# Kernel optimization log

Hardware: AMD Instinct MI355X
Metric: run time of the kernel (lower is better)

## Reference

```python
import jax, jax.numpy as jnp
import numpy as np

B, F, D, H, P, V = 2048, 64, 128, 8, 64, 100000


def setup_inputs() -> dict:
    key = jax.random.key(0)
    ks = jax.random.split(key, 8)
    xavier = lambda k, shape: jax.random.uniform(
        k, shape, jnp.float32, -1.0, 1.0) * np.sqrt(6.0 / (shape[0] + shape[1]))
    return {
        "feat_index": jax.random.randint(ks[0], (B, F), 0, V),
        "emb_table": xavier(ks[1], (V, D)),
        "Wq": xavier(ks[2], (D, H * P)),
        "Wk": xavier(ks[3], (D, H * P)),
        "Wv": xavier(ks[4], (D, H * P)),
        "Wr": xavier(ks[5], (D, H * P)),
        "out_w": xavier(ks[6], (F * H * P, 1)),
        "out_b": jnp.zeros((1,), jnp.float32),
    }


def reference(feat_index, emb_table, Wq, Wk, Wv, Wr, out_w, out_b):
    e = emb_table[feat_index]                                   # [B, F, D]
    # project and split heads: [B, F, H*P] -> [B, H, F, P]
    split = lambda t: t.reshape(B, F, H, P).transpose(0, 2, 1, 3)
    q = split(jnp.einsum('bfd,de->bfe', e, Wq))
    k = split(jnp.einsum('bfd,de->bfe', e, Wk))
    v = split(jnp.einsum('bfd,de->bfe', e, Wv))
    scores = jnp.einsum('bhqp,bhkp->bhqk', q, k)                # [B, H, F, F]
    # NOTE: original applies softmax over dim=2 (the query axis), faithfully kept
    att = jax.nn.softmax(scores, axis=2)
    av = jnp.einsum('bhqk,bhkp->bhqp', att, v)                  # [B, H, F, P]
    # split over heads then cat on last dim == transpose heads next to P
    multi = av.transpose(0, 2, 1, 3).reshape(B, F, H * P)       # [B, F, H*P]
    res = jnp.einsum('bfd,de->bfe', e, Wr)
    multi = jax.nn.relu(multi + res)
    flat = multi.reshape(B, F * H * P)
    y = jax.nn.sigmoid(flat @ out_w + out_b)                    # [B, 1]
    return y
```

## Files before the change

### kernel.cpp

```cpp
#include <hip/hip_runtime.h>
#include <hip/hip_bf16.h>
#include <hip/hip_fp8.h>
#include <stdint.h>


typedef __attribute__((ext_vector_type(8))) __bf16 bf16x8;
typedef __attribute__((ext_vector_type(4))) float f32x4;
typedef __attribute__((ext_vector_type(2))) long long llx2;

#define LDP 72
#define E_SCALE 64.0f
#define W_SCALE 8.0f
#define INV_RAW (1.0f / 512.0f)
#define INV_RAW2 (1.0f / (512.0f * 512.0f))

#define SWZ(row, col) (((row) * 64) + ((col) ^ (((row) & 7) << 3)))

__device__ inline unsigned short f2bf(float f) {
    unsigned u = __float_as_uint(f);
    return (unsigned short)((u + 0x7fff + ((u >> 16) & 1)) >> 16);
}
__device__ inline unsigned short f2bf_t(float f) {
    return (unsigned short)(__float_as_uint(f) >> 16);
}
__device__ inline unsigned pack_bf2(float a, float b) {
#if __has_builtin(__builtin_amdgcn_cvt_pk_bf16_f32)
    typedef __attribute__((ext_vector_type(2))) __bf16 bf16x2;
    bf16x2 r = __builtin_amdgcn_cvt_pk_bf16_f32(a, b);
    return *(unsigned*)&r;
#else
    return (__float_as_uint(a) >> 16) | (__float_as_uint(b) & 0xFFFF0000u);
#endif
}
__device__ inline unsigned pack_fp8x4(float a, float b, float c, float d) {
#if __has_builtin(__builtin_amdgcn_cvt_pk_fp8_f32)
    int u = __builtin_amdgcn_cvt_pk_fp8_f32(a, b, 0, false);
    u = __builtin_amdgcn_cvt_pk_fp8_f32(c, d, u, true);
    return (unsigned)u;
#else
    __hip_fp8_e4m3 qa(a), qb(b), qc(c), qd(d);
    return (unsigned)qa.__x | ((unsigned)qb.__x << 8) |
           ((unsigned)qc.__x << 16) | ((unsigned)qd.__x << 24);
#endif
}

__global__ __launch_bounds__(256) void prep_w(
        const float* __restrict__ Wq, const float* __restrict__ Wk,
        const float* __restrict__ Wv, const float* __restrict__ Wr,
        const float* __restrict__ out_w,
        unsigned char* __restrict__ Wt, float* __restrict__ ow2) {
    int blk = blockIdx.x;
    if (blk >= 256) {
        int i = (blk - 256) * 256 + threadIdx.x;
        int f = i & 63;
        int hp = i >> 6;
        ow2[i] = out_w[(size_t)f * 512 + hp];
        return;
    }
    __shared__ float t[64][20];
    int mat = blk >> 6;
    int dt8 = (blk >> 3) & 7;
    int ct  = blk & 7;
    const float* W = (mat == 0) ? Wq : (mat == 1) ? Wk : (mat == 2) ? Wv : Wr;
    int tid  = threadIdx.x;
    int col  = tid & 63;
    int row0 = tid >> 6;
    for (int i = 0; i < 4; i++) {
        int row = row0 + i * 4;
        t[col][row] = W[(size_t)(dt8 * 16 + row) * 512 + ct * 64 + col];
    }
    __syncthreads();
    int wc  = tid & 63;
    int seg = tid >> 6;
    unsigned u = pack_fp8x4(t[wc][seg * 4 + 0] * W_SCALE, t[wc][seg * 4 + 1] * W_SCALE,
                            t[wc][seg * 4 + 2] * W_SCALE, t[wc][seg * 4 + 3] * W_SCALE);
    int d0 = dt8 * 16 + seg * 4;
    int q_ = (d0 >> 3) & 3, k_ = d0 >> 5, r_ = d0 & 7;
    *(unsigned*)&Wt[((size_t)mat * 512 + ct * 64 + wc) * 128 + q_ * 32 + k_ * 8 + r_] = u;
}

__global__ __launch_bounds__(256, 2) void autoint_kernel(
        const int* __restrict__ fidx,
        const float* __restrict__ emb,
        const unsigned char* __restrict__ Wt,
        const float* __restrict__ ow2,
        const float* __restrict__ out_b,
        float* __restrict__ y) {
    __shared__ __align__(16) unsigned short smem[4 * 64 * 64];
    unsigned short* q_lds   = smem;
    unsigned short* k_lds   = smem + 4096;
    unsigned short* vT_lds  = smem + 2 * 4096;
    unsigned short* att_lds = smem + 3 * 4096;
    unsigned char*  smem8   = (unsigned char*)smem;

    const int b    = blockIdx.x;
    const int tid  = threadIdx.x;
    const int wave = tid >> 6;
    const int lane = tid & 63;
    const int quad = lane >> 4;
    const int ln16 = lane & 15;

    const int* idx = fidx + b * 64;

    for (int it = 0; it < 4; it++) {
        int s  = tid + it * 256;
        int tm = s >> 8, ks = (s >> 6) & 3, qd = (s >> 4) & 3, m = s & 15;
        int f  = tm * 16 + m;
        const float* src = emb + (size_t)idx[f] * 128 + ks * 32 + qd * 8;
        float4 lo = *(const float4*)src;
        float4 hi = *(const float4*)(src + 4);
        uint2 pk;
        pk.x = pack_fp8x4(lo.x * E_SCALE, lo.y * E_SCALE, lo.z * E_SCALE, lo.w * E_SCALE);
        pk.y = pack_fp8x4(hi.x * E_SCALE, hi.y * E_SCALE, hi.z * E_SCALE, hi.w * E_SCALE);
        *(uint2*)&smem8[s * 8] = pk;
    }
    __syncthreads();

    long long a[4][4];
    for (int tm = 0; tm < 4; tm++)
        for (int ks = 0; ks < 4; ks++)
            a[tm][ks] = *(const long long*)&smem8[((tm * 4 + ks) * 64 + lane) * 8];
    __syncthreads();

    float acc_out = 0.f;

    auto loadW = [&](int m, int h, long long (&bf)[4]) {
        const unsigned char* WtM =
            Wt + ((size_t)m * 512 + h * 64 + wave * 16 + ln16) * 128 + quad * 32;
        llx2 w01 = *(const llx2*)WtM;
        llx2 w23 = *(const llx2*)(WtM + 16);
        bf[0] = w01[0]; bf[1] = w01[1]; bf[2] = w23[0]; bf[3] = w23[1];
    };

    auto phase1 = [&](const long long (&bfm)[3][4]) {
        for (int m = 0; m < 3; m++) {
            for (int tm = 0; tm < 4; tm++) {
                f32x4 acc = {0.f, 0.f, 0.f, 0.f};
                __builtin_amdgcn_s_setprio(1);
                for (int ks = 0; ks < 4; ks++)
                    acc = __builtin_amdgcn_mfma_f32_16x16x32_fp8_fp8(a[tm][ks], bfm[m][ks], acc, 0, 0, 0);
                __builtin_amdgcn_s_setprio(0);
                if (m == 0) {
                    for (int r = 0; r < 4; r++)
                        q_lds[SWZ(tm * 16 + quad * 4 + r, wave * 16 + ln16)] = f2bf_t(acc[r]);
                } else if (m == 1) {
                    for (int r = 0; r < 4; r++)
                        k_lds[SWZ(tm * 16 + quad * 4 + r, wave * 16 + ln16)] = f2bf_t(acc[r]);
                } else {
                    uint2 pk;
                    pk.x = pack_bf2(acc[0], acc[1]);
                    pk.y = pack_bf2(acc[2], acc[3]);
                    *(uint2*)&vT_lds[SWZ(wave * 16 + ln16, tm * 16 + quad * 4)] = pk;
                }
            }
        }
    };

    {
        long long bfm[3][4];
        for (int m = 0; m < 3; m++) loadW(m, 0, bfm[m]);
        phase1(bfm);
    }
    __syncthreads();

    for (int h = 0; h < 8; h++) {
        {
            float sc[4][4];
            float sum = 0.f;
            for (int tm = 0; tm < 4; tm++) {
                f32x4 acc = {0.f, 0.f, 0.f, 0.f};
                __builtin_amdgcn_s_setprio(1);
                for (int ks = 0; ks < 2; ks++) {
                    bf16x8 af = *(const bf16x8*)&q_lds[SWZ(tm * 16 + ln16, ks * 32 + quad * 8)];
                    bf16x8 bb = *(const bf16x8*)&k_lds[SWZ(wave * 16 + ln16, ks * 32 + quad * 8)];
                    acc = __builtin_amdgcn_mfma_f32_16x16x32_bf16(af, bb, acc, 0, 0, 0);
                }
                __builtin_amdgcn_s_setprio(0);
                for (int r = 0; r < 4; r++) {
                    float e = __expf(acc[r] * INV_RAW2);
                    sc[tm][r] = e;
                    sum += e;
                }
            }
            sum += __shfl_xor(sum, 16);
            sum += __shfl_xor(sum, 32);
            float inv = 1.f / sum;
            for (int tm = 0; tm < 4; tm++)
                for (int r = 0; r < 4; r++)
                    att_lds[SWZ(tm * 16 + quad * 4 + r, wave * 16 + ln16)] =
                        f2bf_t(sc[tm][r] * inv);
        }
        __syncthreads();

        {
            long long bfr[4];
            loadW(3, h, bfr);
            long long bfn[3][4];
            if (h < 7)
                for (int m = 0; m < 3; m++) loadW(m, h + 1, bfn[m]);
            const float* owr = ow2 + ((size_t)(h * 64 + wave * 16 + ln16)) * 64;
            for (int tm = 0; tm < 4; tm++) {
                float4 owv = *(const float4*)&owr[tm * 16 + quad * 4];
                f32x4 acc = {0.f, 0.f, 0.f, 0.f};
                f32x4 racc = {0.f, 0.f, 0.f, 0.f};
                __builtin_amdgcn_s_setprio(1);
                for (int ks = 0; ks < 2; ks++) {
                    bf16x8 af = *(const bf16x8*)&att_lds[SWZ(tm * 16 + ln16, ks * 32 + quad * 8)];
                    bf16x8 bb = *(const bf16x8*)&vT_lds[SWZ(wave * 16 + ln16, ks * 32 + quad * 8)];
                    acc = __builtin_amdgcn_mfma_f32_16x16x32_bf16(af, bb, acc, 0, 0, 0);
                }
                for (int ks = 0; ks < 4; ks++)
                    racc = __builtin_amdgcn_mfma_f32_16x16x32_fp8_fp8(a[tm][ks], bfr[ks], racc, 0, 0, 0);
                __builtin_amdgcn_s_setprio(0);
                acc_out += fmaxf(acc[0] + racc[0], 0.f) * owv.x;
                acc_out += fmaxf(acc[1] + racc[1], 0.f) * owv.y;
                acc_out += fmaxf(acc[2] + racc[2], 0.f) * owv.z;
                acc_out += fmaxf(acc[3] + racc[3], 0.f) * owv.w;
            }
            if (h < 7) phase1(bfn);
        }
        __syncthreads();
    }

    float* red = (float*)q_lds;
    for (int off = 32; off >= 1; off >>= 1) acc_out += __shfl_xor(acc_out, off);
    if (lane == 0) red[wave] = acc_out;
    __syncthreads();
    if (tid == 0) {
        float s = (red[0] + red[1] + red[2] + red[3]) * INV_RAW + out_b[0];
        y[b] = 1.f / (1.f + __expf(-s));
    }
}

__global__ __launch_bounds__(256) void autoint_kernel_nows(
        const int* __restrict__ fidx,
        const float* __restrict__ emb,
        const float* __restrict__ W0, const float* __restrict__ W1,
        const float* __restrict__ W2, const float* __restrict__ W3,
        const float* __restrict__ out_w, const float* __restrict__ out_b,
        float* __restrict__ y) {
    __shared__ __align__(16) unsigned short escratch[64 * 128];
    __shared__ __align__(16) unsigned short q_lds[64 * LDP];
    __shared__ __align__(16) unsigned short k_lds[64 * LDP];
    __shared__ __align__(16) unsigned short vT_lds[64 * LDP];
    __shared__ float red[4];

    const int b    = blockIdx.x;
    const int tid  = threadIdx.x;
    const int wave = tid >> 6;
    const int lane = tid & 63;
    const int quad = lane >> 4;
    const int ln16 = lane & 15;
    const int* idx = fidx + b * 64;

    for (int it = 0; it < 4; it++) {
        int s  = tid + it * 256;
        int tm = s >> 8, ks = (s >> 6) & 3, qd = (s >> 4) & 3, m = s & 15;
        int f  = tm * 16 + m;
        const float* src = emb + (size_t)idx[f] * 128 + ks * 32 + qd * 8;
        float4 lo = *(const float4*)src;
        float4 hi = *(const float4*)(src + 4);
        uint4 pk;
        pk.x = pack_bf2(lo.x, lo.y); pk.y = pack_bf2(lo.z, lo.w);
        pk.z = pack_bf2(hi.x, hi.y); pk.w = pack_bf2(hi.z, hi.w);
        *(uint4*)&escratch[s * 8] = pk;
    }
    __syncthreads();

    bf16x8 a[4][4];
    for (int tm = 0; tm < 4; tm++)
        for (int ks = 0; ks < 4; ks++)
            a[tm][ks] = *(const bf16x8*)&escratch[((tm * 4 + ks) * 64 + lane) * 8];
    unsigned short* att_lds = escratch;

    float acc_out = 0.f;
    f32x4 r_reg[4];

    for (int h = 0; h < 8; h++) {
        for (int m = 0; m < 4; m++) {
            const float* Wsel = (m == 0) ? W0 : (m == 1) ? W1 : (m == 2) ? W2 : W3;
            bf16x8 bf[4];
            for (int ks = 0; ks < 4; ks++) {
                union { unsigned short u[8]; bf16x8 v; } p;
                const float* base = Wsel + (size_t)(ks * 32 + quad * 8) * 512
                                    + h * 64 + wave * 16 + ln16;
                for (int j = 0; j < 8; j++) p.u[j] = f2bf(base[(size_t)j * 512]);
                bf[ks] = p.v;
            }
            for (int tm = 0; tm < 4; tm++) {
                f32x4 acc = {0.f, 0.f, 0.f, 0.f};
                for (int ks = 0; ks < 4; ks++)
                    acc = __builtin_amdgcn_mfma_f32_16x16x32_bf16(a[tm][ks], bf[ks], acc, 0, 0, 0);
                if (m == 0) {
                    for (int r = 0; r < 4; r++)
                        q_lds[(tm * 16 + quad * 4 + r) * LDP + wave * 16 + ln16] = f2bf_t(acc[r]);
                } else if (m == 1) {
                    for (int r = 0; r < 4; r++)
                        k_lds[(tm * 16 + quad * 4 + r) * LDP + wave * 16 + ln16] = f2bf_t(acc[r]);
                } else if (m == 2) {
                    uint2 pk;
                    pk.x = pack_bf2(acc[0], acc[1]);
                    pk.y = pack_bf2(acc[2], acc[3]);
                    *(uint2*)&vT_lds[(wave * 16 + ln16) * LDP + tm * 16 + quad * 4] = pk;
                } else {
                    r_reg[tm] = acc;
                }
            }
        }
        __syncthreads();
        {
            float sc[4][4];
            float sum = 0.f;
            for (int tm = 0; tm < 4; tm++) {
                f32x4 acc = {0.f, 0.f, 0.f, 0.f};
                for (int ks = 0; ks < 2; ks++) {
                    bf16x8 af = *(const bf16x8*)&q_lds[(tm * 16 + ln16) * LDP + ks * 32 + quad * 8];
                    bf16x8 bb = *(const bf16x8*)&k_lds[(wave * 16 + ln16) * LDP + ks * 32 + quad * 8];
                    acc = __builtin_amdgcn_mfma_f32_16x16x32_bf16(af, bb, acc, 0, 0, 0);
                }
                for (int r = 0; r < 4; r++) {
                    float e = __expf(acc[r]);
                    sc[tm][r] = e;
                    sum += e;
                }
            }
            sum += __shfl_xor(sum, 16);
            sum += __shfl_xor(sum, 32);
            float inv = 1.f / sum;
            for (int tm = 0; tm < 4; tm++)
                for (int r = 0; r < 4; r++)
                    att_lds[(tm * 16 + quad * 4 + r) * LDP + wave * 16 + ln16] =
                        f2bf_t(sc[tm][r] * inv);
        }
        __syncthreads();
        {
            const float* ow = out_w + h * 64 + wave * 16;
            for (int tm = 0; tm < 4; tm++) {
                f32x4 acc = {0.f, 0.f, 0.f, 0.f};
                for (int ks = 0; ks < 2; ks++) {
                    bf16x8 af = *(const bf16x8*)&att_lds[(tm * 16 + ln16) * LDP + ks * 32 + quad * 8];
                    bf16x8 bb = *(const bf16x8*)&vT_lds[(wave * 16 + ln16) * LDP + ks * 32 + quad * 8];
                    acc = __builtin_amdgcn_mfma_f32_16x16x32_bf16(af, bb, acc, 0, 0, 0);
                }
                for (int r = 0; r < 4; r++) {
                    int f = tm * 16 + quad * 4 + r;
                    float mval = acc[r] + r_reg[tm][r];
                    if (mval > 0.f) acc_out += mval * ow[(size_t)f * 512 + ln16];
                }
            }
        }
        __syncthreads();
    }
    for (int off = 32; off >= 1; off >>= 1) acc_out += __shfl_xor(acc_out, off);
    if (lane == 0) red[wave] = acc_out;
    __syncthreads();
    if (tid == 0) {
        float s = red[0] + red[1] + red[2] + red[3] + out_b[0];
        y[b] = 1.f / (1.f + __expf(-s));
    }
}

extern "C" void kernel_launch(void* const* d_in, const int* in_sizes, int n_in,
                              void* d_out, int out_size, void* d_ws, size_t ws_size,
                              hipStream_t stream) {
    (void)in_sizes; (void)n_in; (void)out_size;
    const int*   fidx = (const int*)d_in[0];
    const float* emb  = (const float*)d_in[1];
    const float* Wq   = (const float*)d_in[2];
    const float* Wk   = (const float*)d_in[3];
    const float* Wv   = (const float*)d_in[4];
    const float* Wr   = (const float*)d_in[5];
    const float* ow   = (const float*)d_in[6];
    const float* ob   = (const float*)d_in[7];
    float*       yy   = (float*)d_out;

    const size_t wt_bytes  = (size_t)4 * 512 * 128;
    const size_t ow2_bytes = (size_t)8 * 64 * 64 * 4;
    if (d_ws != nullptr && ws_size >= wt_bytes + ow2_bytes) {
        unsigned char* Wt  = (unsigned char*)d_ws;
        float*         ow2 = (float*)((unsigned char*)d_ws + wt_bytes);
        prep_w<<<384, 256, 0, stream>>>(Wq, Wk, Wv, Wr, ow, Wt, ow2);
        autoint_kernel<<<2048, 256, 0, stream>>>(fidx, emb, Wt, ow2, ob, yy);
    } else {
        autoint_kernel_nows<<<2048, 256, 0, stream>>>(fidx, emb, Wq, Wk, Wv, Wr, ow, ob, yy);
    }
}
```

Baseline: 203.5 us.

## Process two batch rows per workgroup to amortize weight loads and barriers

```diff
diff --git a/kernel.cpp b/kernel.cpp
--- a/kernel.cpp
+++ b/kernel.cpp
@@ -15,6 +15,11 @@
 #define INV_RAW2 (1.0f / (512.0f * 512.0f))
 
 #define SWZ(row, col) (((row) * 64) + ((col) ^ (((row) & 7) << 3)))
+
+#define QL(j)  (smem + (j) * 16384)
+#define KL(j)  (smem + (j) * 16384 + 4096)
+#define VTL(j) (smem + (j) * 16384 + 8192)
+#define ATL(j) (smem + (j) * 16384 + 12288)
 
 __device__ inline unsigned short f2bf(float f) {
     unsigned u = __float_as_uint(f);
@@ -86,43 +91,46 @@
         const float* __restrict__ ow2,
         const float* __restrict__ out_b,
         float* __restrict__ y) {
-    __shared__ __align__(16) unsigned short smem[4 * 64 * 64];
-    unsigned short* q_lds   = smem;
-    unsigned short* k_lds   = smem + 4096;
-    unsigned short* vT_lds  = smem + 2 * 4096;
-    unsigned short* att_lds = smem + 3 * 4096;
-    unsigned char*  smem8   = (unsigned char*)smem;
-
-    const int b    = blockIdx.x;
+    __shared__ __align__(16) unsigned short smem[8 * 4096];
+    unsigned char* smem8 = (unsigned char*)smem;
+
+    const int b2   = blockIdx.x;
     const int tid  = threadIdx.x;
     const int wave = tid >> 6;
     const int lane = tid & 63;
     const int quad = lane >> 4;
     const int ln16 = lane & 15;
 
-    const int* idx = fidx + b * 64;
-
-    for (int it = 0; it < 4; it++) {
+    const int* idx0 = fidx + (size_t)(2 * b2) * 64;
+    const int* idx1 = idx0 + 64;
+
+    for (int it = 0; it < 8; it++) {
         int s  = tid + it * 256;
-        int tm = s >> 8, ks = (s >> 6) & 3, qd = (s >> 4) & 3, m = s & 15;
+        int j  = s >> 10;
+        int ss = s & 1023;
+        int tm = ss >> 8, ks = (ss >> 6) & 3, qd = (ss >> 4) & 3, m = ss & 15;
         int f  = tm * 16 + m;
+        const int* idx = j ? idx1 : idx0;
         const float* src = emb + (size_t)idx[f] * 128 + ks * 32 + qd * 8;
         float4 lo = *(const float4*)src;
         float4 hi = *(const float4*)(src + 4);
         uint2 pk;
         pk.x = pack_fp8x4(lo.x * E_SCALE, lo.y * E_SCALE, lo.z * E_SCALE, lo.w * E_SCALE);
         pk.y = pack_fp8x4(hi.x * E_SCALE, hi.y * E_SCALE, hi.z * E_SCALE, hi.w * E_SCALE);
-        *(uint2*)&smem8[s * 8] = pk;
-    }
-    __syncthreads();
-
-    long long a[4][4];
-    for (int tm = 0; tm < 4; tm++)
-        for (int ks = 0; ks < 4; ks++)
-            a[tm][ks] = *(const long long*)&smem8[((tm * 4 + ks) * 64 + lane) * 8];
-    __syncthreads();
-
-    float acc_out = 0.f;
+        *(uint2*)&smem8[j * 32768 + ss * 8] = pk;
+    }
+    __syncthreads();
+
+    long long a[2][4][4];
+#pragma unroll
+    for (int j = 0; j < 2; j++)
+        for (int tm = 0; tm < 4; tm++)
+            for (int ks = 0; ks < 4; ks++)
+                a[j][tm][ks] =
+                    *(const long long*)&smem8[j * 32768 + ((tm * 4 + ks) * 64 + lane) * 8];
+    __syncthreads();
+
+    float acc_out[2] = {0.f, 0.f};
 
     auto loadW = [&](int m, int h, long long (&bf)[4]) {
         const unsigned char* WtM =
@@ -132,13 +140,16 @@
         bf[0] = w01[0]; bf[1] = w01[1]; bf[2] = w23[0]; bf[3] = w23[1];
     };
 
-    auto phase1 = [&](const long long (&bfm)[3][4]) {
+    auto phase1 = [&](const long long (&bfm)[3][4], int j) {
+        unsigned short* q_lds  = QL(j);
+        unsigned short* k_lds  = KL(j);
+        unsigned short* vT_lds = VTL(j);
         for (int m = 0; m < 3; m++) {
             for (int tm = 0; tm < 4; tm++) {
                 f32x4 acc = {0.f, 0.f, 0.f, 0.f};
                 __builtin_amdgcn_s_setprio(1);
                 for (int ks = 0; ks < 4; ks++)
-                    acc = __builtin_amdgcn_mfma_f32_16x16x32_fp8_fp8(a[tm][ks], bfm[m][ks], acc, 0, 0, 0);
+                    acc = __builtin_amdgcn_mfma_f32_16x16x32_fp8_fp8(a[j][tm][ks], bfm[m][ks], acc, 0, 0, 0);
                 __builtin_amdgcn_s_setprio(0);
                 if (m == 0) {
                     for (int r = 0; r < 4; r++)
@@ -156,40 +167,47 @@
         }
     };
 
+    auto phase2 = [&](int j) {
+        unsigned short* q_lds   = QL(j);
+        unsigned short* k_lds   = KL(j);
+        unsigned short* att_lds = ATL(j);
+        float sc[4][4];
+        float sum = 0.f;
+        for (int tm = 0; tm < 4; tm++) {
+            f32x4 acc = {0.f, 0.f, 0.f, 0.f};
+            __builtin_amdgcn_s_setprio(1);
+            for (int ks = 0; ks < 2; ks++) {
+                bf16x8 af = *(const bf16x8*)&q_lds[SWZ(tm * 16 + ln16, ks * 32 + quad * 8)];
+                bf16x8 bb = *(const bf16x8*)&k_lds[SWZ(wave * 16 + ln16, ks * 32 + quad * 8)];
+                acc = __builtin_amdgcn_mfma_f32_16x16x32_bf16(af, bb, acc, 0, 0, 0);
+            }
+            __builtin_amdgcn_s_setprio(0);
+            for (int r = 0; r < 4; r++) {
+                float e = __expf(acc[r] * INV_RAW2);
+                sc[tm][r] = e;
+                sum += e;
+            }
+        }
+        sum += __shfl_xor(sum, 16);
+        sum += __shfl_xor(sum, 32);
+        float inv = 1.f / sum;
+        for (int tm = 0; tm < 4; tm++)
+            for (int r = 0; r < 4; r++)
+                att_lds[SWZ(tm * 16 + quad * 4 + r, wave * 16 + ln16)] =
+                    f2bf_t(sc[tm][r] * inv);
+    };
+
     {
         long long bfm[3][4];
         for (int m = 0; m < 3; m++) loadW(m, 0, bfm[m]);
-        phase1(bfm);
+        phase1(bfm, 0);
+        phase1(bfm, 1);
     }
     __syncthreads();
 
     for (int h = 0; h < 8; h++) {
-        {
-            float sc[4][4];
-            float sum = 0.f;
-            for (int tm = 0; tm < 4; tm++) {
-                f32x4 acc = {0.f, 0.f, 0.f, 0.f};
-                __builtin_amdgcn_s_setprio(1);
-                for (int ks = 0; ks < 2; ks++) {
-                    bf16x8 af = *(const bf16x8*)&q_lds[SWZ(tm * 16 + ln16, ks * 32 + quad * 8)];
-                    bf16x8 bb = *(const bf16x8*)&k_lds[SWZ(wave * 16 + ln16, ks * 32 + quad * 8)];
-                    acc = __builtin_amdgcn_mfma_f32_16x16x32_bf16(af, bb, acc, 0, 0, 0);
-                }
-                __builtin_amdgcn_s_setprio(0);
-                for (int r = 0; r < 4; r++) {
-                    float e = __expf(acc[r] * INV_RAW2);
-                    sc[tm][r] = e;
-                    sum += e;
-                }
-            }
-            sum += __shfl_xor(sum, 16);
-            sum += __shfl_xor(sum, 32);
-            float inv = 1.f / sum;
-            for (int tm = 0; tm < 4; tm++)
-                for (int r = 0; r < 4; r++)
-                    att_lds[SWZ(tm * 16 + quad * 4 + r, wave * 16 + ln16)] =
-                        f2bf_t(sc[tm][r] * inv);
-        }
+        phase2(0);
+        phase2(1);
         __syncthreads();
 
         {
@@ -201,34 +219,45 @@
             const float* owr = ow2 + ((size_t)(h * 64 + wave * 16 + ln16)) * 64;
             for (int tm = 0; tm < 4; tm++) {
                 float4 owv = *(const float4*)&owr[tm * 16 + quad * 4];
-                f32x4 acc = {0.f, 0.f, 0.f, 0.f};
-                f32x4 racc = {0.f, 0.f, 0.f, 0.f};
-                __builtin_amdgcn_s_setprio(1);
-                for (int ks = 0; ks < 2; ks++) {
-                    bf16x8 af = *(const bf16x8*)&att_lds[SWZ(tm * 16 + ln16, ks * 32 + quad * 8)];
-                    bf16x8 bb = *(const bf16x8*)&vT_lds[SWZ(wave * 16 + ln16, ks * 32 + quad * 8)];
-                    acc = __builtin_amdgcn_mfma_f32_16x16x32_bf16(af, bb, acc, 0, 0, 0);
-                }
-                for (int ks = 0; ks < 4; ks++)
-                    racc = __builtin_amdgcn_mfma_f32_16x16x32_fp8_fp8(a[tm][ks], bfr[ks], racc, 0, 0, 0);
-                __builtin_amdgcn_s_setprio(0);
-                acc_out += fmaxf(acc[0] + racc[0], 0.f) * owv.x;
-                acc_out += fmaxf(acc[1] + racc[1], 0.f) * owv.y;
-                acc_out += fmaxf(acc[2] + racc[2], 0.f) * owv.z;
-                acc_out += fmaxf(acc[3] + racc[3], 0.f) * owv.w;
-            }
-            if (h < 7) phase1(bfn);
+#pragma unroll
+                for (int j = 0; j < 2; j++) {
+                    const unsigned short* att_lds = ATL(j);
+                    const unsigned short* vT_lds  = VTL(j);
+                    f32x4 acc = {0.f, 0.f, 0.f, 0.f};
+                    f32x4 racc = {0.f, 0.f, 0.f, 0.f};
+                    __builtin_amdgcn_s_setprio(1);
+                    for (int ks = 0; ks < 2; ks++) {
+                        bf16x8 af = *(const bf16x8*)&att_lds[SWZ(tm * 16 + ln16, ks * 32 + quad * 8)];
+                        bf16x8 bb = *(const bf16x8*)&vT_lds[SWZ(wave * 16 + ln16, ks * 32 + quad * 8)];
+                        acc = __builtin_amdgcn_mfma_f32_16x16x32_bf16(af, bb, acc, 0, 0, 0);
+                    }
+                    for (int ks = 0; ks < 4; ks++)
+                        racc = __builtin_amdgcn_mfma_f32_16x16x32_fp8_fp8(a[j][tm][ks], bfr[ks], racc, 0, 0, 0);
+                    __builtin_amdgcn_s_setprio(0);
+                    acc_out[j] += fmaxf(acc[0] + racc[0], 0.f) * owv.x;
+                    acc_out[j] += fmaxf(acc[1] + racc[1], 0.f) * owv.y;
+                    acc_out[j] += fmaxf(acc[2] + racc[2], 0.f) * owv.z;
+                    acc_out[j] += fmaxf(acc[3] + racc[3], 0.f) * owv.w;
+                }
+            }
+            if (h < 7) { phase1(bfn, 0); phase1(bfn, 1); }
         }
         __syncthreads();
     }
 
-    float* red = (float*)q_lds;
-    for (int off = 32; off >= 1; off >>= 1) acc_out += __shfl_xor(acc_out, off);
-    if (lane == 0) red[wave] = acc_out;
-    __syncthreads();
-    if (tid == 0) {
-        float s = (red[0] + red[1] + red[2] + red[3]) * INV_RAW + out_b[0];
-        y[b] = 1.f / (1.f + __expf(-s));
+    float* red = (float*)QL(0);
+#pragma unroll
+    for (int j = 0; j < 2; j++) {
+        float v = acc_out[j];
+        for (int off = 32; off >= 1; off >>= 1) v += __shfl_xor(v, off);
+        if (lane == 0) red[j * 4 + wave] = v;
+    }
+    __syncthreads();
+    if (tid < 2) {
+        int j = tid;
+        float s = (red[j * 4 + 0] + red[j * 4 + 1] + red[j * 4 + 2] + red[j * 4 + 3])
+                      * INV_RAW + out_b[0];
+        y[2 * b2 + j] = 1.f / (1.f + __expf(-s));
     }
 }
 
@@ -380,7 +409,7 @@
         unsigned char* Wt  = (unsigned char*)d_ws;
         float*         ow2 = (float*)((unsigned char*)d_ws + wt_bytes);
         prep_w<<<384, 256, 0, stream>>>(Wq, Wk, Wv, Wr, ow, Wt, ow2);
-        autoint_kernel<<<2048, 256, 0, stream>>>(fidx, emb, Wt, ow2, ob, yy);
+        autoint_kernel<<<1024, 256, 0, stream>>>(fidx, emb, Wt, ow2, ob, yy);
     } else {
         autoint_kernel_nows<<<2048, 256, 0, stream>>>(fidx, emb, Wq, Wk, Wv, Wr, ow, ob, yy);
     }
```

New measurement: 192.0 us. 5.6% less time.
